# Kernel tuning notes

Hardware: AMD Instinct MI355X
Metric: run time of the kernel (lower is better)

Reference implementation:

```python
import jax, jax.numpy as jnp
import numpy as np

D = 1024
H = 16
DK = D // H
EPS = 1e-5


def _layernorm(x, g, b):
    mu = jnp.mean(x, axis=-1, keepdims=True)
    var = jnp.var(x, axis=-1, keepdims=True)
    return (x - mu) * jax.lax.rsqrt(var + EPS) * g + b


def setup_inputs() -> dict:
    key = jax.random.key(0)
    ks = jax.random.split(key, 8)
    N, T = 4, 2048
    # module initializes Wqkv/Wout with torch.randn (std=1); mimic that scale
    x = jax.random.normal(ks[0], (N, T, D), dtype=jnp.float32)
    mask = jnp.zeros((N, 1, 1, T), dtype=jnp.float32)  # additive padding mask
    Wqkv = jax.random.normal(ks[1], (D, 3 * D), dtype=jnp.float32)
    Wout = jax.random.normal(ks[2], (D, D), dtype=jnp.float32)
    ln1_g = jnp.ones((D,), jnp.float32); ln1_b = jnp.zeros((D,), jnp.float32)
    ln2_g = jnp.ones((D,), jnp.float32); ln2_b = jnp.zeros((D,), jnp.float32)
    s1 = (1.0 / np.sqrt(D)); s2 = (1.0 / np.sqrt(4 * D))
    W1 = jax.random.uniform(ks[3], (D, 4 * D), jnp.float32, -s1, s1)
    b1 = jnp.zeros((4 * D,), jnp.float32)
    W2 = jax.random.uniform(ks[4], (4 * D, D), jnp.float32, -s2, s2)
    b2 = jnp.zeros((D,), jnp.float32)
    return dict(x=x, mask=mask, Wqkv=Wqkv, Wout=Wout, ln1_g=ln1_g, ln1_b=ln1_b,
                ln2_g=ln2_g, ln2_b=ln2_b, W1=W1, b1=b1, W2=W2, b2=b2)


def reference(x, mask, Wqkv, Wout, ln1_g, ln1_b, ln2_g, ln2_b, W1, b1, W2, b2):
    N, T, _ = x.shape
    # --- attention sublayer: Residual(PreNorm(MHSA)) ---
    z = _layernorm(x, ln1_g, ln1_b)
    qkv = z @ Wqkv  # [N,T,3D]
    Q, K, V = jnp.split(qkv, 3, axis=-1)
    Q, K, V = [a.reshape(N, T, H, DK).swapaxes(1, 2) for a in (Q, K, V)]  # [N,H,T,dk]
    scores = jnp.einsum('nhtd,nhsd->nhts', Q, K) * (DK ** -0.5) + mask
    attn = jax.nn.softmax(scores, axis=-1)  # dropout in eval mode = identity
    ctx = jnp.einsum('nhts,nhsd->nhtd', attn, V)
    attn_out = ctx.swapaxes(1, 2).reshape(N, T, D) @ Wout
    x = x + attn_out
    # --- FFN sublayer: Residual(PreNorm(FFN)), exact (erf) GELU ---
    z = _layernorm(x, ln2_g, ln2_b)
    h = jax.nn.gelu(z @ W1 + b1, approximate=False)
    x = x + (h @ W2 + b2)
    return x
```

## Files before the change

kernel.cpp:

```cpp
#include <hip/hip_runtime.h>
#include <math.h>

#define DEV __device__ __forceinline__

typedef short bf16x8 __attribute__((ext_vector_type(8)));
typedef float f32x4 __attribute__((ext_vector_type(4)));

DEV float bf2f(short s){
  union{ float f; unsigned u; } v; v.u = ((unsigned)(unsigned short)s) << 16; return v.f;
}
DEV short f2b(float f){
  union{ float f; unsigned u; } v; v.f = f;
  unsigned r = v.u + 0x7fffu + ((v.u >> 16) & 1u);
  return (short)(r >> 16);
}
DEV unsigned pk2(float a, float b){
  return ((unsigned)(unsigned short)f2b(b) << 16) | (unsigned short)f2b(a);
}
DEV unsigned pk2t(float a, float b){
  union{ float f; unsigned u; } ua, ub; ua.f = a; ub.f = b;
  return __builtin_amdgcn_perm(ub.u, ua.u, 0x07060302);
}

DEV void gll16(const void* g, void* l){
  __builtin_amdgcn_global_load_lds((const __attribute__((address_space(1))) void*)g,
                                   (__attribute__((address_space(3))) void*)l, 16, 0, 0);
}

template<bool SPLIT>
__global__ void tsplit_kernel(const float* __restrict__ in, short* __restrict__ hi,
                              short* __restrict__ lo, int R, int C){
  __shared__ float tile[32][33];
  int tc = blockIdx.x*32, tr = blockIdx.y*32;
  int lx = threadIdx.x, ly = threadIdx.y;
  for (int i = 0; i < 32; i += 8)
    tile[ly+i][lx] = in[(size_t)(tr+ly+i)*C + tc+lx];
  __syncthreads();
  for (int i = 0; i < 32; i += 8){
    float v = tile[lx][ly+i];
    size_t o = (size_t)(tc+ly+i)*R + tr+lx;
    short h_ = f2b(v); hi[o] = h_;
    if constexpr (SPLIT) lo[o] = f2b(v - bf2f(h_));
  }
}

template<bool SPLIT>
__global__ void ln_kernel(const float* __restrict__ x, const float* __restrict__ g,
                          const float* __restrict__ bta, short* __restrict__ hi,
                          short* __restrict__ lo){
  int row = blockIdx.x, tid = threadIdx.x;
  const float* xr = x + (size_t)row*1024;
  float v[4], s = 0.f, q = 0.f;
  #pragma unroll
  for (int i = 0; i < 4; i++){ v[i] = xr[tid + i*256]; s += v[i]; q += v[i]*v[i]; }
  #pragma unroll
  for (int m = 1; m < 64; m <<= 1){ s += __shfl_xor(s, m); q += __shfl_xor(q, m); }
  __shared__ float red[8];
  int wave = tid >> 6, lane = tid & 63;
  if (lane == 0){ red[wave] = s; red[4+wave] = q; }
  __syncthreads();
  s = red[0]+red[1]+red[2]+red[3];
  q = red[4]+red[5]+red[6]+red[7];
  float mu = s * (1.f/1024.f);
  float var = q * (1.f/1024.f) - mu*mu;
  float rstd = rsqrtf(var + 1e-5f);
  #pragma unroll
  for (int i = 0; i < 4; i++){
    int d = tid + i*256;
    float z = (v[i]-mu)*rstd*g[d] + bta[d];
    short h_ = f2b(z);
    hi[(size_t)row*1024 + d] = h_;
    if constexpr (SPLIT) lo[(size_t)row*1024 + d] = f2b(z - bf2f(h_));
  }
}

constexpr int BM = 128, BN = 128, BK = 32;

template<int MODE, bool SPLIT>
__global__ __launch_bounds__(256, 2) void gemm_kernel(
    const short* __restrict__ Ahi, const short* __restrict__ Alo,
    const short* __restrict__ Bhi, const short* __restrict__ Blo,
    int M, int N, int K,
    float* __restrict__ outf, short* __restrict__ outb,
    const float* __restrict__ res, const float* __restrict__ bias,
    short* __restrict__ qhi, short* __restrict__ qlo,
    short* __restrict__ khi, short* __restrict__ klo,
    short* __restrict__ vbf)
{
  __shared__ short lds[(SPLIT ? 4 : 2) * BM * BK];
  short* sAhi = lds;
  short* sBhi = lds + BM*BK;
  short* sAlo = lds;
  short* sBlo = lds;
  if constexpr (SPLIT){ sAlo = lds + 2*BM*BK; sBlo = lds + 3*BM*BK; }

  const int tid = threadIdx.x;
  const int wave = tid >> 6, lane = tid & 63;
  const int bm = blockIdx.y * BM, bn = blockIdx.x * BN;
  const int wm = (wave >> 1) * 64, wn = (wave & 1) * 64;

  f32x4 acc[4][4] = {};

  const int srow = lane >> 2;
  const int skq  = (lane & 3) * 8;

  for (int k0 = 0; k0 < K; k0 += BK){
    #pragma unroll
    for (int i = 0; i < 2; i++){
      int seg = wave*2 + i;
      int row = seg*16 + srow;
      gll16(Ahi + (size_t)(bm+row)*K + k0 + skq, sAhi + seg*16*BK);
      gll16(Bhi + (size_t)(bn+row)*K + k0 + skq, sBhi + seg*16*BK);
      if constexpr (SPLIT){
        gll16(Alo + (size_t)(bm+row)*K + k0 + skq, sAlo + seg*16*BK);
        gll16(Blo + (size_t)(bn+row)*K + k0 + skq, sBlo + seg*16*BK);
      }
    }
    __syncthreads();
    bf16x8 ah[4], bh[4], al[4], bl[4];
    #pragma unroll
    for (int i = 0; i < 4; i++){
      int ra = (wm + i*16 + (lane & 15)) * BK + (lane >> 4) * 8;
      int rb = (wn + i*16 + (lane & 15)) * BK + (lane >> 4) * 8;
      ah[i] = *(const bf16x8*)&sAhi[ra];
      bh[i] = *(const bf16x8*)&sBhi[rb];
      if constexpr (SPLIT){
        al[i] = *(const bf16x8*)&sAlo[ra];
        bl[i] = *(const bf16x8*)&sBlo[rb];
      }
    }
    __syncthreads();
    #pragma unroll
    for (int i = 0; i < 4; i++)
      #pragma unroll
      for (int j = 0; j < 4; j++){
        acc[i][j] = __builtin_amdgcn_mfma_f32_16x16x32_bf16(ah[i], bh[j], acc[i][j], 0, 0, 0);
        if constexpr (SPLIT){
          acc[i][j] = __builtin_amdgcn_mfma_f32_16x16x32_bf16(ah[i], bl[j], acc[i][j], 0, 0, 0);
          acc[i][j] = __builtin_amdgcn_mfma_f32_16x16x32_bf16(al[i], bh[j], acc[i][j], 0, 0, 0);
        }
      }
  }

  const int row0 = bm + wm + (lane >> 4) * 4;
  const int col0 = bn + wn + (lane & 15);
  #pragma unroll
  for (int i = 0; i < 4; i++)
    #pragma unroll
    for (int j = 0; j < 4; j++){
      int col = col0 + j*16;
      #pragma unroll
      for (int r = 0; r < 4; r++){
        int row = row0 + i*16 + r;
        float v = acc[i][j][r];
        if constexpr (MODE == 1){
          size_t o = (size_t)row*N + col;
          outf[o] = res[o] + v;
        } else if constexpr (MODE == 2){
          float t = v + bias[col];
          t = 0.5f * t * (1.0f + erff(t * 0.70710678118654752f));
          outb[(size_t)row*N + col] = f2b(t);
        } else if constexpr (MODE == 3){
          size_t o = (size_t)row*N + col;
          outf[o] = res[o] + v + bias[col];
        } else if constexpr (MODE == 4){
          int nb = row >> 11, tt = row & 2047;
          int hh = col >> 6, dk = col & 63;
          vbf[((size_t)(nb*16 + hh)*64 + dk)*2048 + tt] = f2b(v);
        } else {
          int nb = row >> 11, tt = row & 2047;
          if (col < 1024){
            int h = col >> 6, dk = col & 63;
            size_t o = ((size_t)(nb*16 + h)*2048 + tt)*64 + dk;
            float vq = v * 0.125f;
            short h_ = f2b(vq); qhi[o] = h_; qlo[o] = f2b(vq - bf2f(h_));
          } else {
            int c = col - 1024, h = c >> 6, dk = c & 63;
            size_t o = ((size_t)(nb*16 + h)*2048 + tt)*64 + dk;
            short h_ = f2b(v); khi[o] = h_; klo[o] = f2b(v - bf2f(h_));
          }
        }
      }
    }
}

__global__ __launch_bounds__(512, 4) void attn_kernel(
    const short* __restrict__ qhi, const short* __restrict__ qlo,
    const short* __restrict__ khi, const short* __restrict__ klo,
    const short* __restrict__ vt,  const float* __restrict__ mask,
    short* __restrict__ ctx)
{
  __shared__ short lds[3*128*64];
  short* sKh = lds;
  short* sKl = lds + 8192;
  short* sV  = lds + 16384;
  short* sQh = sKh;
  short* sQl = sKl;

  const int tid = threadIdx.x, wave = tid >> 6, lane = tid & 63;
  const int qd = lane >> 4, n16 = lane & 15;
  const int nh = blockIdx.x, nb = nh >> 4, h = nh & 15;
  const int q0 = blockIdx.y * 128;
  const size_t qoff = ((size_t)nh*2048 + q0)*64;
  const int sw = n16 & 7;

  {
    int cg = ((lane & 7) ^ (lane >> 3)) * 8;
    int rowl = lane >> 3;
    #pragma unroll
    for (int i = 0; i < 2; i++){
      int seg = wave*2 + i;
      int row = seg*8 + rowl;
      gll16(qhi + qoff + (size_t)row*64 + cg, sQh + seg*512);
      gll16(qlo + qoff + (size_t)row*64 + cg, sQl + seg*512);
    }
  }
  __syncthreads();

  bf16x8 bqh[2], bql[2];
  #pragma unroll
  for (int k2 = 0; k2 < 2; k2++){
    int off = (wave*16 + n16)*64 + (((k2*4 + qd) ^ sw) << 3);
    bqh[k2] = *(const bf16x8*)&sQh[off];
    bql[k2] = *(const bf16x8*)&sQl[off];
  }

  float m_i = -1e30f, l_i = 0.f;
  f32x4 o_[4] = {};
  short* myP = lds + wave*2048;
  const float4* mask4 = (const float4*)(mask + (size_t)nb*2048);

  for (int kt = 0; kt < 2048; kt += 128){
    __syncthreads();
    const size_t koff = ((size_t)nh*2048 + kt)*64;
    {
      int cg = ((lane & 7) ^ (lane >> 3)) * 8;
      int rowl = lane >> 3;
      #pragma unroll
      for (int i = 0; i < 2; i++){
        int seg = wave*2 + i;
        int row = seg*8 + rowl;
        gll16(khi + koff + (size_t)row*64 + cg, sKh + seg*512);
        gll16(klo + koff + (size_t)row*64 + cg, sKl + seg*512);
      }
      #pragma unroll
      for (int i = 0; i < 2; i++){
        int seg = wave*2 + i;
        int dk = seg*4 + qd;
        int cgv = ((lane & 15) ^ (dk & 7)) * 8;
        gll16(vt + ((size_t)nh*64 + dk)*2048 + kt + cgv, sV + seg*512);
      }
    }
    __syncthreads();

    f32x4 sc[8];
    #pragma unroll
    for (int j = 0; j < 8; j++){
      f32x4 z = {};
      #pragma unroll
      for (int k2 = 0; k2 < 2; k2++){
        int off = (j*16 + n16)*64 + (((k2*4 + qd) ^ sw) << 3);
        bf16x8 akh = *(const bf16x8*)&sKh[off];
        bf16x8 akl = *(const bf16x8*)&sKl[off];
        z = __builtin_amdgcn_mfma_f32_16x16x32_bf16(akh, bqh[k2], z, 0, 0, 0);
        z = __builtin_amdgcn_mfma_f32_16x16x32_bf16(akh, bql[k2], z, 0, 0, 0);
        z = __builtin_amdgcn_mfma_f32_16x16x32_bf16(akl, bqh[k2], z, 0, 0, 0);
      }
      sc[j] = z;
    }

    float mloc = -1e30f;
    #pragma unroll
    for (int j = 0; j < 8; j++){
      float4 mk = mask4[(kt >> 2) + j*4 + qd];
      const float* mkp = (const float*)&mk;
      #pragma unroll
      for (int r = 0; r < 4; r++){
        float s = sc[j][r] + mkp[r];
        sc[j][r] = s;
        mloc = fmaxf(mloc, s);
      }
    }
    mloc = fmaxf(mloc, __shfl_xor(mloc, 16, 64));
    mloc = fmaxf(mloc, __shfl_xor(mloc, 32, 64));
    float mnew = fmaxf(m_i, mloc);
    float alpha = __expf(m_i - mnew);
    m_i = mnew;
    float ps = 0.f;
    #pragma unroll
    for (int j = 0; j < 8; j++)
      #pragma unroll
      for (int r = 0; r < 4; r++){
        float p = __expf(sc[j][r] - mnew);
        sc[j][r] = p;
        ps += p;
      }
    ps += __shfl_xor(ps, 16, 64);
    ps += __shfl_xor(ps, 32, 64);
    l_i = l_i*alpha + ps;
    #pragma unroll
    for (int c = 0; c < 4; c++)
      #pragma unroll
      for (int r = 0; r < 4; r++) o_[c][r] *= alpha;

    __syncthreads();

    #pragma unroll
    for (int b = 0; b < 8; b++){
      uint2 w;
      w.x = pk2t(sc[b][0], sc[b][1]);
      w.y = pk2t(sc[b][2], sc[b][3]);
      int off = n16*128 + ((((b*2 + (qd >> 1)) ^ sw)) << 3) + (qd & 1)*4;
      *(uint2*)&myP[off] = w;
    }

    #pragma unroll
    for (int kq = 0; kq < 4; kq++){
      bf16x8 bp = *(const bf16x8*)&myP[n16*128 + (((kq*4 + qd) ^ sw) << 3)];
      #pragma unroll
      for (int c = 0; c < 4; c++){
        bf16x8 av = *(const bf16x8*)&sV[(c*16 + n16)*128 + (((kq*4 + qd) ^ sw) << 3)];
        o_[c] = __builtin_amdgcn_mfma_f32_16x16x32_bf16(av, bp, o_[c], 0, 0, 0);
      }
    }
  }

  float linv = 1.0f / l_i;
  int row = q0 + wave*16 + n16;
  size_t base = ((size_t)nb*2048 + row)*1024 + h*64;
  #pragma unroll
  for (int c = 0; c < 4; c++){
    uint2 w;
    w.x = pk2(o_[c][0]*linv, o_[c][1]*linv);
    w.y = pk2(o_[c][2]*linv, o_[c][3]*linv);
    *(uint2*)&ctx[base + c*16 + qd*4] = w;
  }
}

extern "C" void kernel_launch(void* const* d_in, const int* in_sizes, int n_in,
                              void* d_out, int out_size, void* d_ws, size_t ws_size,
                              hipStream_t stream)
{
  (void)in_sizes; (void)n_in; (void)out_size; (void)ws_size;
  const float* x    = (const float*)d_in[0];
  const float* mask = (const float*)d_in[1];
  const float* Wqkv = (const float*)d_in[2];
  const float* Wout = (const float*)d_in[3];
  const float* ln1g = (const float*)d_in[4];
  const float* ln1b = (const float*)d_in[5];
  const float* ln2g = (const float*)d_in[6];
  const float* ln2b = (const float*)d_in[7];
  const float* W1   = (const float*)d_in[8];
  const float* b1   = (const float*)d_in[9];
  const float* W2   = (const float*)d_in[10];
  const float* b2   = (const float*)d_in[11];
  float* out = (float*)d_out;

  const int M = 8192;
  const size_t MB = 1024*1024;
  char* ws = (char*)d_ws;

  short* wqT_h = (short*)(ws + 0*MB);
  short* wqT_l = (short*)(ws + 6*MB);
  short* zhi   = (short*)(ws + 12*MB);
  short* zlo   = (short*)(ws + 28*MB);
  short* qh    = (short*)(ws + 44*MB);
  short* ql    = (short*)(ws + 60*MB);
  short* kh    = (short*)(ws + 76*MB);
  short* kl    = (short*)(ws + 92*MB);
  short* vb    = (short*)(ws + 108*MB);
  short* ctx   = (short*)(ws + 0*MB);
  short* woT   = (short*)(ws + 16*MB);
  float* x2    = (float*)(ws + 64*MB);
  short* z2    = (short*)(ws + 96*MB);
  short* w1T   = (short*)(ws + 112*MB);
  short* w2T   = (short*)(ws + 120*MB);
  short* hbuf  = (short*)(ws + 0*MB);

  dim3 tb(32, 8);

  tsplit_kernel<true ><<<dim3(3072/32, 1024/32), tb, 0, stream>>>(Wqkv, wqT_h, wqT_l, 1024, 3072);
  ln_kernel<true ><<<dim3(M), dim3(256), 0, stream>>>(x, ln1g, ln1b, zhi, zlo);

  gemm_kernel<0, true><<<dim3(2048/128, M/128), dim3(256), 0, stream>>>(
      zhi, zlo, wqT_h, wqT_l, M, 2048, 1024,
      nullptr, nullptr, nullptr, nullptr,
      qh, ql, kh, kl, nullptr);

  gemm_kernel<4, false><<<dim3(1024/128, M/128), dim3(256), 0, stream>>>(
      zhi, nullptr, wqT_h + (size_t)2048*1024, nullptr, M, 1024, 1024,
      nullptr, nullptr, nullptr, nullptr,
      nullptr, nullptr, nullptr, nullptr, vb);

  tsplit_kernel<false><<<dim3(1024/32, 1024/32), tb, 0, stream>>>(Wout, woT, nullptr, 1024, 1024);

  attn_kernel<<<dim3(64, 2048/128), dim3(512), 0, stream>>>(qh, ql, kh, kl, vb, mask, ctx);

  tsplit_kernel<false><<<dim3(4096/32, 1024/32), tb, 0, stream>>>(W1, w1T, nullptr, 1024, 4096);
  tsplit_kernel<false><<<dim3(1024/32, 4096/32), tb, 0, stream>>>(W2, w2T, nullptr, 4096, 1024);

  gemm_kernel<1, false><<<dim3(1024/128, M/128), dim3(256), 0, stream>>>(
      ctx, nullptr, woT, nullptr, M, 1024, 1024,
      x2, nullptr, x, nullptr,
      nullptr, nullptr, nullptr, nullptr, nullptr);

  ln_kernel<false><<<dim3(M), dim3(256), 0, stream>>>(x2, ln2g, ln2b, z2, nullptr);

  gemm_kernel<2, false><<<dim3(4096/128, M/128), dim3(256), 0, stream>>>(
      z2, nullptr, w1T, nullptr, M, 4096, 1024,
      nullptr, hbuf, nullptr, b1,
      nullptr, nullptr, nullptr, nullptr, nullptr);

  gemm_kernel<3, false><<<dim3(1024/128, M/128), dim3(256), 0, stream>>>(
      hbuf, nullptr, w2T, nullptr, M, 1024, 4096,
      out, nullptr, x2, b2,
      nullptr, nullptr, nullptr, nullptr, nullptr);
}
```

Before: 684.2 us.

## Use exp2 softmax, fp16 PV, BK=64 GEMMs, sigmoid GELU, merged transposes

Folds log2e into the Q scale and a pre-scaled mask so attention can use exp2. P and V are stored as fp16 and multiplied with f16 MFMA. The single-precision GEMMs move to a K-tile of 64 to halve barrier count per K. Weight transpose launches are merged pairwise, and exact erf GELU is replaced with a sigmoid-based approximation, which trades accuracy for cheaper epilogue math.

```diff
diff --git a/kernel.cpp b/kernel.cpp
--- a/kernel.cpp
+++ b/kernel.cpp
@@ -5,6 +5,8 @@
 
 typedef short bf16x8 __attribute__((ext_vector_type(8)));
 typedef float f32x4 __attribute__((ext_vector_type(4)));
+typedef _Float16 f16x8 __attribute__((ext_vector_type(8)));
+typedef __fp16 h16x2 __attribute__((ext_vector_type(2)));
 
 DEV float bf2f(short s){
   union{ float f; unsigned u; } v; v.u = ((unsigned)(unsigned short)s) << 16; return v.f;
@@ -17,9 +19,13 @@
 DEV unsigned pk2(float a, float b){
   return ((unsigned)(unsigned short)f2b(b) << 16) | (unsigned short)f2b(a);
 }
-DEV unsigned pk2t(float a, float b){
-  union{ float f; unsigned u; } ua, ub; ua.f = a; ub.f = b;
-  return __builtin_amdgcn_perm(ub.u, ua.u, 0x07060302);
+DEV unsigned pkh2(float a, float b){
+  union{ h16x2 h; unsigned u; } x;
+  x.h = __builtin_amdgcn_cvt_pkrtz(a, b);
+  return x.u;
+}
+DEV short f2h(float f){
+  union{ _Float16 h; short s; } u; u.h = (_Float16)f; return u.s;
 }
 
 DEV void gll16(const void* g, void* l){
@@ -27,11 +33,18 @@
                                    (__attribute__((address_space(3))) void*)l, 16, 0, 0);
 }
 
-template<bool SPLIT>
-__global__ void tsplit_kernel(const float* __restrict__ in, short* __restrict__ hi,
-                              short* __restrict__ lo, int R, int C){
+__global__ void tsplit2_kernel(const float* __restrict__ inA, short* __restrict__ hiA,
+                               short* __restrict__ loA, int RA, int CA,
+                               const float* __restrict__ inB, short* __restrict__ hiB,
+                               short* __restrict__ loB, int RB, int CB){
   __shared__ float tile[32][33];
-  int tc = blockIdx.x*32, tr = blockIdx.y*32;
+  int ntA = (RA >> 5) * (CA >> 5);
+  int t = blockIdx.x;
+  const float* in; short* hi; short* lo; int R, C;
+  if (t < ntA){ in = inA; hi = hiA; lo = loA; R = RA; C = CA; }
+  else { t -= ntA; in = inB; hi = hiB; lo = loB; R = RB; C = CB; }
+  int cx = C >> 5;
+  int tc = (t % cx) * 32, tr = (t / cx) * 32;
   int lx = threadIdx.x, ly = threadIdx.y;
   for (int i = 0; i < 32; i += 8)
     tile[ly+i][lx] = in[(size_t)(tr+ly+i)*C + tc+lx];
@@ -40,14 +53,15 @@
     float v = tile[lx][ly+i];
     size_t o = (size_t)(tc+ly+i)*R + tr+lx;
     short h_ = f2b(v); hi[o] = h_;
-    if constexpr (SPLIT) lo[o] = f2b(v - bf2f(h_));
+    if (lo) lo[o] = f2b(v - bf2f(h_));
   }
 }
 
 template<bool SPLIT>
 __global__ void ln_kernel(const float* __restrict__ x, const float* __restrict__ g,
                           const float* __restrict__ bta, short* __restrict__ hi,
-                          short* __restrict__ lo){
+                          short* __restrict__ lo,
+                          const float* __restrict__ msrc, float* __restrict__ mdst){
   int row = blockIdx.x, tid = threadIdx.x;
   const float* xr = x + (size_t)row*1024;
   float v[4], s = 0.f, q = 0.f;
@@ -72,11 +86,12 @@
     hi[(size_t)row*1024 + d] = h_;
     if constexpr (SPLIT) lo[(size_t)row*1024 + d] = f2b(z - bf2f(h_));
   }
-}
-
-constexpr int BM = 128, BN = 128, BK = 32;
-
-template<int MODE, bool SPLIT>
+  if (msrc && tid == 0) mdst[row] = msrc[row] * 1.44269504089f;
+}
+
+constexpr int BM = 128, BN = 128;
+
+template<int MODE, bool SPLIT, int BK>
 __global__ __launch_bounds__(256, 2) void gemm_kernel(
     const short* __restrict__ Ahi, const short* __restrict__ Alo,
     const short* __restrict__ Bhi, const short* __restrict__ Blo,
@@ -96,54 +111,61 @@
 
   const int tid = threadIdx.x;
   const int wave = tid >> 6, lane = tid & 63;
+  const int n16 = lane & 15, qd = lane >> 4;
   const int bm = blockIdx.y * BM, bn = blockIdx.x * BN;
   const int wm = (wave >> 1) * 64, wn = (wave & 1) * 64;
 
   f32x4 acc[4][4] = {};
 
-  const int srow = lane >> 2;
-  const int skq  = (lane & 3) * 8;
+  constexpr int CPR = BK / 8;
+  constexpr int IPW = BK / 16;
+  constexpr int RPI = 512 / BK;
+  const int srow = lane / CPR;
+  const int skq  = (lane % CPR) * 8;
 
   for (int k0 = 0; k0 < K; k0 += BK){
     #pragma unroll
-    for (int i = 0; i < 2; i++){
-      int seg = wave*2 + i;
-      int row = seg*16 + srow;
-      gll16(Ahi + (size_t)(bm+row)*K + k0 + skq, sAhi + seg*16*BK);
-      gll16(Bhi + (size_t)(bn+row)*K + k0 + skq, sBhi + seg*16*BK);
+    for (int i = 0; i < IPW; i++){
+      int seg = wave*IPW + i;
+      int row = seg*RPI + srow;
+      gll16(Ahi + (size_t)(bm+row)*K + k0 + skq, sAhi + seg*512);
+      gll16(Bhi + (size_t)(bn+row)*K + k0 + skq, sBhi + seg*512);
       if constexpr (SPLIT){
-        gll16(Alo + (size_t)(bm+row)*K + k0 + skq, sAlo + seg*16*BK);
-        gll16(Blo + (size_t)(bn+row)*K + k0 + skq, sBlo + seg*16*BK);
+        gll16(Alo + (size_t)(bm+row)*K + k0 + skq, sAlo + seg*512);
+        gll16(Blo + (size_t)(bn+row)*K + k0 + skq, sBlo + seg*512);
       }
     }
     __syncthreads();
-    bf16x8 ah[4], bh[4], al[4], bl[4];
-    #pragma unroll
-    for (int i = 0; i < 4; i++){
-      int ra = (wm + i*16 + (lane & 15)) * BK + (lane >> 4) * 8;
-      int rb = (wn + i*16 + (lane & 15)) * BK + (lane >> 4) * 8;
-      ah[i] = *(const bf16x8*)&sAhi[ra];
-      bh[i] = *(const bf16x8*)&sBhi[rb];
-      if constexpr (SPLIT){
-        al[i] = *(const bf16x8*)&sAlo[ra];
-        bl[i] = *(const bf16x8*)&sBlo[rb];
-      }
+    #pragma unroll
+    for (int kk = 0; kk < BK/32; kk++){
+      bf16x8 ah[4], bh[4], al[4], bl[4];
+      #pragma unroll
+      for (int i = 0; i < 4; i++){
+        int ra = (wm + i*16 + n16) * BK + kk*32 + qd*8;
+        int rb = (wn + i*16 + n16) * BK + kk*32 + qd*8;
+        ah[i] = *(const bf16x8*)&sAhi[ra];
+        bh[i] = *(const bf16x8*)&sBhi[rb];
+        if constexpr (SPLIT){
+          al[i] = *(const bf16x8*)&sAlo[ra];
+          bl[i] = *(const bf16x8*)&sBlo[rb];
+        }
+      }
+      #pragma unroll
+      for (int i = 0; i < 4; i++)
+        #pragma unroll
+        for (int j = 0; j < 4; j++){
+          acc[i][j] = __builtin_amdgcn_mfma_f32_16x16x32_bf16(ah[i], bh[j], acc[i][j], 0, 0, 0);
+          if constexpr (SPLIT){
+            acc[i][j] = __builtin_amdgcn_mfma_f32_16x16x32_bf16(ah[i], bl[j], acc[i][j], 0, 0, 0);
+            acc[i][j] = __builtin_amdgcn_mfma_f32_16x16x32_bf16(al[i], bh[j], acc[i][j], 0, 0, 0);
+          }
+        }
     }
     __syncthreads();
-    #pragma unroll
-    for (int i = 0; i < 4; i++)
-      #pragma unroll
-      for (int j = 0; j < 4; j++){
-        acc[i][j] = __builtin_amdgcn_mfma_f32_16x16x32_bf16(ah[i], bh[j], acc[i][j], 0, 0, 0);
-        if constexpr (SPLIT){
-          acc[i][j] = __builtin_amdgcn_mfma_f32_16x16x32_bf16(ah[i], bl[j], acc[i][j], 0, 0, 0);
-          acc[i][j] = __builtin_amdgcn_mfma_f32_16x16x32_bf16(al[i], bh[j], acc[i][j], 0, 0, 0);
-        }
-      }
-  }
-
-  const int row0 = bm + wm + (lane >> 4) * 4;
-  const int col0 = bn + wn + (lane & 15);
+  }
+
+  const int row0 = bm + wm + qd * 4;
+  const int col0 = bn + wn + n16;
   #pragma unroll
   for (int i = 0; i < 4; i++)
     #pragma unroll
@@ -158,21 +180,21 @@
           outf[o] = res[o] + v;
         } else if constexpr (MODE == 2){
           float t = v + bias[col];
-          t = 0.5f * t * (1.0f + erff(t * 0.70710678118654752f));
-          outb[(size_t)row*N + col] = f2b(t);
+          float g = t / (1.0f + exp2f(-2.4554669f * t));
+          outb[(size_t)row*N + col] = f2b(g);
         } else if constexpr (MODE == 3){
           size_t o = (size_t)row*N + col;
           outf[o] = res[o] + v + bias[col];
         } else if constexpr (MODE == 4){
           int nb = row >> 11, tt = row & 2047;
           int hh = col >> 6, dk = col & 63;
-          vbf[((size_t)(nb*16 + hh)*64 + dk)*2048 + tt] = f2b(v);
+          vbf[((size_t)(nb*16 + hh)*64 + dk)*2048 + tt] = f2h(v);
         } else {
           int nb = row >> 11, tt = row & 2047;
           if (col < 1024){
             int h = col >> 6, dk = col & 63;
             size_t o = ((size_t)(nb*16 + h)*2048 + tt)*64 + dk;
-            float vq = v * 0.125f;
+            float vq = v * 0.18033988749f;
             short h_ = f2b(vq); qhi[o] = h_; qlo[o] = f2b(vq - bf2f(h_));
           } else {
             int c = col - 1024, h = c >> 6, dk = c & 63;
@@ -284,14 +306,14 @@
     mloc = fmaxf(mloc, __shfl_xor(mloc, 16, 64));
     mloc = fmaxf(mloc, __shfl_xor(mloc, 32, 64));
     float mnew = fmaxf(m_i, mloc);
-    float alpha = __expf(m_i - mnew);
+    float alpha = exp2f(m_i - mnew);
     m_i = mnew;
     float ps = 0.f;
     #pragma unroll
     for (int j = 0; j < 8; j++)
       #pragma unroll
       for (int r = 0; r < 4; r++){
-        float p = __expf(sc[j][r] - mnew);
+        float p = exp2f(sc[j][r] - mnew);
         sc[j][r] = p;
         ps += p;
       }
@@ -308,19 +330,19 @@
     #pragma unroll
     for (int b = 0; b < 8; b++){
       uint2 w;
-      w.x = pk2t(sc[b][0], sc[b][1]);
-      w.y = pk2t(sc[b][2], sc[b][3]);
+      w.x = pkh2(sc[b][0], sc[b][1]);
+      w.y = pkh2(sc[b][2], sc[b][3]);
       int off = n16*128 + ((((b*2 + (qd >> 1)) ^ sw)) << 3) + (qd & 1)*4;
       *(uint2*)&myP[off] = w;
     }
 
     #pragma unroll
     for (int kq = 0; kq < 4; kq++){
-      bf16x8 bp = *(const bf16x8*)&myP[n16*128 + (((kq*4 + qd) ^ sw) << 3)];
+      f16x8 bp = *(const f16x8*)&myP[n16*128 + (((kq*4 + qd) ^ sw) << 3)];
       #pragma unroll
       for (int c = 0; c < 4; c++){
-        bf16x8 av = *(const bf16x8*)&sV[(c*16 + n16)*128 + (((kq*4 + qd) ^ sw) << 3)];
-        o_[c] = __builtin_amdgcn_mfma_f32_16x16x32_bf16(av, bp, o_[c], 0, 0, 0);
+        f16x8 av = *(const f16x8*)&sV[(c*16 + n16)*128 + (((kq*4 + qd) ^ sw) << 3)];
+        o_[c] = __builtin_amdgcn_mfma_f32_16x16x32_f16(av, bp, o_[c], 0, 0, 0);
       }
     }
   }
@@ -369,8 +391,9 @@
   short* kh    = (short*)(ws + 76*MB);
   short* kl    = (short*)(ws + 92*MB);
   short* vb    = (short*)(ws + 108*MB);
+  short* woT   = (short*)(ws + 124*MB);
+  float* mask2 = (float*)(ws + 127*MB);
   short* ctx   = (short*)(ws + 0*MB);
-  short* woT   = (short*)(ws + 16*MB);
   float* x2    = (float*)(ws + 64*MB);
   short* z2    = (short*)(ws + 96*MB);
   short* w1T   = (short*)(ws + 112*MB);
@@ -379,39 +402,40 @@
 
   dim3 tb(32, 8);
 
-  tsplit_kernel<true ><<<dim3(3072/32, 1024/32), tb, 0, stream>>>(Wqkv, wqT_h, wqT_l, 1024, 3072);
-  ln_kernel<true ><<<dim3(M), dim3(256), 0, stream>>>(x, ln1g, ln1b, zhi, zlo);
-
-  gemm_kernel<0, true><<<dim3(2048/128, M/128), dim3(256), 0, stream>>>(
+  tsplit2_kernel<<<dim3(3072 + 1024), tb, 0, stream>>>(
+      Wqkv, wqT_h, wqT_l, 1024, 3072,  Wout, woT, nullptr, 1024, 1024);
+
+  ln_kernel<true ><<<dim3(M), dim3(256), 0, stream>>>(x, ln1g, ln1b, zhi, zlo, mask, mask2);
+
+  gemm_kernel<0, true, 32><<<dim3(2048/128, M/128), dim3(256), 0, stream>>>(
       zhi, zlo, wqT_h, wqT_l, M, 2048, 1024,
       nullptr, nullptr, nullptr, nullptr,
       qh, ql, kh, kl, nullptr);
 
-  gemm_kernel<4, false><<<dim3(1024/128, M/128), dim3(256), 0, stream>>>(
+  gemm_kernel<4, false, 64><<<dim3(1024/128, M/128), dim3(256), 0, stream>>>(
       zhi, nullptr, wqT_h + (size_t)2048*1024, nullptr, M, 1024, 1024,
       nullptr, nullptr, nullptr, nullptr,
       nullptr, nullptr, nullptr, nullptr, vb);
 
-  tsplit_kernel<false><<<dim3(1024/32, 1024/32), tb, 0, stream>>>(Wout, woT, nullptr, 1024, 1024);
-
-  attn_kernel<<<dim3(64, 2048/128), dim3(512), 0, stream>>>(qh, ql, kh, kl, vb, mask, ctx);
-
-  tsplit_kernel<false><<<dim3(4096/32, 1024/32), tb, 0, stream>>>(W1, w1T, nullptr, 1024, 4096);
-  tsplit_kernel<false><<<dim3(1024/32, 4096/32), tb, 0, stream>>>(W2, w2T, nullptr, 4096, 1024);
-
-  gemm_kernel<1, false><<<dim3(1024/128, M/128), dim3(256), 0, stream>>>(
+  attn_kernel<<<dim3(64, 2048/128), dim3(512), 0, stream>>>(qh, ql, kh, kl, vb, mask2, ctx);
+
+  gemm_kernel<1, false, 64><<<dim3(1024/128, M/128), dim3(256), 0, stream>>>(
       ctx, nullptr, woT, nullptr, M, 1024, 1024,
       x2, nullptr, x, nullptr,
       nullptr, nullptr, nullptr, nullptr, nullptr);
 
-  ln_kernel<false><<<dim3(M), dim3(256), 0, stream>>>(x2, ln2g, ln2b, z2, nullptr);
-
-  gemm_kernel<2, false><<<dim3(4096/128, M/128), dim3(256), 0, stream>>>(
+  tsplit2_kernel<<<dim3(4096 + 4096), tb, 0, stream>>>(
+      W1, w1T, nullptr, 1024, 4096,  W2, w2T, nullptr, 4096, 1024);
+
+  ln_kernel<false><<<dim3(M), dim3(256), 0, stream>>>(x2, ln2g, ln2b, z2, nullptr,
+                                                      nullptr, nullptr);
+
+  gemm_kernel<2, false, 64><<<dim3(4096/128, M/128), dim3(256), 0, stream>>>(
       z2, nullptr, w1T, nullptr, M, 4096, 1024,
       nullptr, hbuf, nullptr, b1,
       nullptr, nullptr, nullptr, nullptr, nullptr);
 
-  gemm_kernel<3, false><<<dim3(1024/128, M/128), dim3(256), 0, stream>>>(
+  gemm_kernel<3, false, 64><<<dim3(1024/128, M/128), dim3(256), 0, stream>>>(
       hbuf, nullptr, w2T, nullptr, M, 1024, 4096,
       out, nullptr, x2, b2,
       nullptr, nullptr, nullptr, nullptr, nullptr);
```

After: 689.3 us. Within noise of the previous version (+0.8%).
